# Kernel tuning notes

Hardware: AMD Instinct MI355X
Metric: run time of the kernel (lower is better)

Reference implementation:

```python
import jax, jax.numpy as jnp
import numpy as np

B = 64
N_CTRL_PLANES = 512
CPD = 64          # control_plane_dim
NF = 256          # n_frames
WS = 512          # window_size (SSM per-frame output size)
SD = 128          # state_dim
NS = NF * WS // 2 # 65536 output samples (overlap-add hop = WS//2)
TOP_K = 8


def setup_inputs() -> dict:
    key = jax.random.key(0)
    ks = jax.random.split(key, 8)
    return {
        "control_plane_choice": jax.random.normal(ks[0], (B, N_CTRL_PLANES), dtype=jnp.float32),
        "times": jax.random.normal(ks[1], (B, 1, NF), dtype=jnp.float32),
        # Lookup.items, initialized uniform(-1, 1)
        "lookup_items": jax.random.uniform(ks[2], (N_CTRL_PLANES, CPD * NF), dtype=jnp.float32, minval=-1.0, maxval=1.0),
        # SSM parameters, initialized uniform(-0.01, 0.01)
        "proj": jax.random.uniform(ks[3], (CPD, WS), dtype=jnp.float32, minval=-0.01, maxval=0.01),
        "state_matrix": jax.random.uniform(ks[4], (SD, SD), dtype=jnp.float32, minval=-0.01, maxval=0.01),
        "input_matrix": jax.random.uniform(ks[5], (WS, SD), dtype=jnp.float32, minval=-0.01, maxval=0.01),
        "output_matrix": jax.random.uniform(ks[6], (SD, WS), dtype=jnp.float32, minval=-0.01, maxval=0.01),
        "direct_matrix": jax.random.uniform(ks[7], (WS, WS), dtype=jnp.float32, minval=-0.01, maxval=0.01),
    }


def _sparse_softmax_onehot(x, axis=-1):
    # softmax then hard one-hot at the argmax with value 1 (normalize=True variant)
    sm = jax.nn.softmax(x, axis=axis)
    return (sm == jnp.max(sm, axis=axis, keepdims=True)).astype(x.dtype)


def _fft_convolve(a, b):
    # linear convolution via zero-padding to 2N, truncated back to N
    n = a.shape[-1]
    fa = jnp.fft.rfft(jnp.pad(a, ((0, 0), (0, 0), (0, n))), axis=-1)
    fb = jnp.fft.rfft(jnp.pad(b, ((0, 0), (0, 0), (0, n))), axis=-1)
    return jnp.fft.irfft(fa * fb, axis=-1)[..., :n]


def reference(control_plane_choice, times, lookup_items, proj, state_matrix, input_matrix, output_matrix, direct_matrix):
    batch = control_plane_choice.shape[0]
    cpd, ws = proj.shape
    nf = lookup_items.shape[1] // cpd
    sd = state_matrix.shape[0]
    hop = ws // 2
    ns = nf * hop

    # --- Lookup with sparse_softmax selection (hard one-hot @ items) ---
    sel = _sparse_softmax_onehot(control_plane_choice, axis=-1)   # (B, n_items)
    cp = sel @ lookup_items                                       # (B, cpd*nf)

    # --- softmax over flattened control plane, then top-8 sparsify ---
    cp = jax.nn.softmax(cp, axis=-1)                              # (B, cpd*nf)
    vals, idx = jax.lax.top_k(cp, TOP_K)                          # (B, 8)
    cp = jnp.zeros_like(cp).at[jnp.arange(batch)[:, None], idx].set(vals)
    cp = cp.reshape(batch, cpd, nf)

    # --- windowed SSM: linear state-space recurrence over frames ---
    inp = jnp.einsum('bcf,cw->fbw', cp, proj)                     # (nf, B, ws)

    def step(state, x):  # state: (B, sd), x: (B, ws)
        state = state @ state_matrix + x @ input_matrix
        out = state @ output_matrix + x @ direct_matrix
        return state, out

    state0 = jnp.zeros((batch, sd), dtype=cp.dtype)
    _, outs = jax.lax.scan(step, state0, inp)                     # (nf, B, ws)
    frames = jnp.transpose(outs, (1, 0, 2))                       # (B, nf, ws)

    # --- overlap-add with Hann window, hop = ws//2 ---
    n_ = jnp.arange(ws, dtype=cp.dtype)
    window = 0.5 * (1.0 - jnp.cos(2.0 * jnp.pi * n_ / ws))        # periodic Hann
    win_frames = frames * window
    oa_idx = jnp.arange(nf)[:, None] * hop + jnp.arange(ws)[None, :]
    sig = jnp.zeros((batch, nf * hop + ws), dtype=cp.dtype).at[:, oa_idx].add(win_frames)
    samples = sig[:, :ns][:, None, :]                             # (B, 1, ns)

    # --- Dirac scheduler: one-hot times -> upsample with holes -> fft convolve ---
    t_oh = _sparse_softmax_onehot(times, axis=-1)                 # (B, 1, nf)
    factor = ns // nf
    impulses = jnp.zeros((batch, 1, ns), dtype=cp.dtype).at[:, :, ::factor].set(t_oh)
    return _fft_convolve(samples, impulses)                       # (B, 1, ns)
```

## Files before the change

### kernel.cpp

```cpp
#include <hip/hip_runtime.h>
#include <math.h>

#define NBATCH 64
#define NCP    512
#define CPD    64
#define NF     256
#define WSZ    512
#define SD     128
#define NSAMP  65536
#define TPROP  8
#define NSLICE 8
#define SLICE_ELEMS 2048

__device__ __forceinline__ bool better(float v1, int i1, float v2, int i2) {
  return (v1 > v2) || (v1 == v2 && i1 < i2);
}

__device__ __forceinline__ void cswap(float& v1, int& i1, float& v2, int& i2) {
  if (better(v2, i2, v1, i1)) {
    float tv = v1; v1 = v2; v2 = tv;
    int   ti = i1; i1 = i2; i2 = ti;
  }
}

__device__ __forceinline__ void wave_argmax(float& v, int& i) {
#pragma unroll
  for (int off = 32; off > 0; off >>= 1) {
    float ov = __shfl_down(v, off);
    int   oi = __shfl_down(i, off);
    if (better(ov, oi, v, i)) { v = ov; i = oi; }
  }
}

__device__ __forceinline__ void xor_merge8(float* m, int* mi, int off) {
  float lb[8]; int ib8[8];
#pragma unroll
  for (int k = 0; k < 8; k++) { lb[k] = __shfl_xor(m[k], off); ib8[k] = __shfl_xor(mi[k], off); }
  float x[8]; int xi[8];
#pragma unroll
  for (int k = 0; k < 8; k++) {
    const bool ta = better(m[k], mi[k], lb[7 - k], ib8[7 - k]);
    x[k]  = ta ? m[k]  : lb[7 - k];
    xi[k] = ta ? mi[k] : ib8[7 - k];
  }
  cswap(x[0], xi[0], x[4], xi[4]); cswap(x[1], xi[1], x[5], xi[5]);
  cswap(x[2], xi[2], x[6], xi[6]); cswap(x[3], xi[3], x[7], xi[7]);
  cswap(x[0], xi[0], x[2], xi[2]); cswap(x[1], xi[1], x[3], xi[3]);
  cswap(x[4], xi[4], x[6], xi[6]); cswap(x[5], xi[5], x[7], xi[7]);
  cswap(x[0], xi[0], x[1], xi[1]); cswap(x[2], xi[2], x[3], xi[3]);
  cswap(x[4], xi[4], x[5], xi[5]); cswap(x[6], xi[6], x[7], xi[7]);
#pragma unroll
  for (int k = 0; k < 8; k++) { m[k] = x[k]; mi[k] = xi[k]; }
}

__global__ __launch_bounds__(256) void k_scan(
    const float* __restrict__ cpc, const float* __restrict__ times,
    const float* __restrict__ lookup,
    const float* __restrict__ proj, const float* __restrict__ Amat,
    const float* __restrict__ Bmat,
    float* __restrict__ S,
    float* __restrict__ pmax, float* __restrict__ psum,
    float* __restrict__ pcv, int* __restrict__ pci,
    int* __restrict__ pshift) {
  const int t = threadIdx.x;
  const int bid = blockIdx.x;

  __shared__ __align__(16) float Alds[SD * SD];
  __shared__ float sb[2][SD];
  __shared__ float sred[256];
  __shared__ float wred[4];
  __shared__ int   wredi[4];
  __shared__ int   sRow;
  __shared__ float wlv[32];
  __shared__ int   wli[32];
  __shared__ float sSmax;

  if (bid < CPD) {
    const int c = bid;
    for (int i = t; i < SD * SD / 4; i += 256)
      ((float4*)Alds)[i] = ((const float4*)Amat)[i];

    const int d = t & 127, h = t >> 7;
    {
      const float* Bp = Bmat + (size_t)(h * 256) * SD + d;
      const float* pv = proj + (size_t)c * WSZ + h * 256;
      float acc[16];
#pragma unroll
      for (int k = 0; k < 16; k++) acc[k] = 0.f;
#pragma unroll 2
      for (int kb = 0; kb < 256; kb += 16) {
#pragma unroll
        for (int u = 0; u < 16; u++)
          acc[u] = fmaf(pv[kb + u], Bp[(size_t)(kb + u) * SD], acc[u]);
      }
      float s8 = 0.f;
#pragma unroll
      for (int k = 0; k < 16; k++) s8 += acc[k];
      sred[t] = s8;
    }
    __syncthreads();
    if (t < SD) sb[0][t] = sred[t] + sred[t + 128];
    __syncthreads();

    int cur = 0;
    for (int j = 0; j < TPROP; j++) {
      if (t < SD) S[((size_t)j * CPD + c) * SD + t] = sb[cur][t];
      float a0 = 0.f, a1 = 0.f, a2 = 0.f, a3 = 0.f;
      const float* Ah = Alds + (size_t)(h * 64) * SD + d;
      const float* sh = sb[cur] + h * 64;
#pragma unroll
      for (int i = 0; i < 64; i += 4) {
        const float4 sv = *(const float4*)(sh + i);
        a0 = fmaf(sv.x, Ah[(size_t)(i + 0) * SD], a0);
        a1 = fmaf(sv.y, Ah[(size_t)(i + 1) * SD], a1);
        a2 = fmaf(sv.z, Ah[(size_t)(i + 2) * SD], a2);
        a3 = fmaf(sv.w, Ah[(size_t)(i + 3) * SD], a3);
      }
      sred[t] = (a0 + a1) + (a2 + a3);
      __syncthreads();
      if (t < SD) sb[cur ^ 1][t] = sred[t] + sred[t + 128];
      __syncthreads();
      cur ^= 1;
    }
    return;
  }

  const int sbid = bid - CPD;
  const int b = sbid >> 3, s = sbid & 7;
  const int lane = t & 63, wv = t >> 6;

  {
    float v0 = cpc[b * NCP + t];
    float v1 = cpc[b * NCP + t + 256];
    float bv = v0; int bi = t;
    if (better(v1, t + 256, bv, bi)) { bv = v1; bi = t + 256; }
    wave_argmax(bv, bi);
    if (lane == 0) { wred[wv] = bv; wredi[wv] = bi; }
    __syncthreads();
    if (t == 0) {
      float fv = wred[0]; int fi = wredi[0];
#pragma unroll
      for (int q = 1; q < 4; q++)
        if (better(wred[q], wredi[q], fv, fi)) { fv = wred[q]; fi = wredi[q]; }
      sRow = fi;
    }
    __syncthreads();
  }
  const float* row = lookup + (size_t)sRow * (CPD * NF);
  const float4* row4 = (const float4*)(row + s * SLICE_ELEMS);

  const float4 va = row4[t];
  const float4 vb = row4[t + 256];
  const int gbase = s * SLICE_ELEMS;
  float ev[8] = {va.x, va.y, va.z, va.w, vb.x, vb.y, vb.z, vb.w};
  int   ei[8] = {gbase + t * 4,        gbase + t * 4 + 1,
                 gbase + t * 4 + 2,    gbase + t * 4 + 3,
                 gbase + 1024 + t * 4, gbase + 1024 + t * 4 + 1,
                 gbase + 1024 + t * 4 + 2, gbase + 1024 + t * 4 + 3};

  float m[8]; int mi[8];
#pragma unroll
  for (int k = 0; k < 8; k++) { m[k] = ev[k]; mi[k] = ei[k]; }
#pragma unroll
  for (int i = 0; i < 7; i++)
#pragma unroll
    for (int j = 0; j < 7 - i; j++) cswap(m[j], mi[j], m[j + 1], mi[j + 1]);

  xor_merge8(m, mi, 1);  xor_merge8(m, mi, 2);  xor_merge8(m, mi, 4);
  xor_merge8(m, mi, 8);  xor_merge8(m, mi, 16); xor_merge8(m, mi, 32);

  if (lane < 8) { wlv[wv * 8 + lane] = m[lane]; wli[wv * 8 + lane] = mi[lane]; }
  __syncthreads();

  if (wv == 0) {
    float v = (lane < 32) ? wlv[lane] : -3.4e38f;
    int   i = (lane < 32) ? wli[lane] : 0x7fffffff;
#pragma unroll
    for (int k = 2; k <= 32; k <<= 1) {
#pragma unroll
      for (int j = k >> 1; j > 0; j >>= 1) {
        const float pv = __shfl_xor(v, j);
        const int   pi = __shfl_xor(i, j);
        const bool keepBetter = (((lane & k) == 0) == ((lane & j) == 0));
        if (keepBetter == better(pv, pi, v, i)) { v = pv; i = pi; }
      }
    }
    if (lane == 0) sSmax = v;
    if (lane < 8) { pcv[b * 64 + s * 8 + lane] = v; pci[b * 64 + s * 8 + lane] = i; }
  }
  __syncthreads();
  const float smax = sSmax;

  float se = 0.f;
#pragma unroll
  for (int k = 0; k < 8; k++) se += __expf(ev[k] - smax);
#pragma unroll
  for (int off = 32; off > 0; off >>= 1) se += __shfl_down(se, off);
  if (lane == 0) wred[wv] = se;
  __syncthreads();
  if (t == 0) {
    pmax[b * 8 + s] = smax;
    psum[b * 8 + s] = (wred[0] + wred[1]) + (wred[2] + wred[3]);
  }

  if (s == 0) {
    float tv = times[b * NF + t]; int ti = t;
    wave_argmax(tv, ti);
    if (lane == 0) { wred[wv] = tv; wredi[wv] = ti; }
    __syncthreads();
    if (t == 0) {
      float fv = wred[0]; int fi = wredi[0];
#pragma unroll
      for (int q = 1; q < 4; q++)
        if (better(wred[q], wredi[q], fv, fi)) { fv = wred[q]; fi = wredi[q]; }
      pshift[b] = fi * (NSAMP / NF);
    }
  }
}

__global__ __launch_bounds__(256) void k_expand(
    const float* __restrict__ proj, const float* __restrict__ Cmat,
    const float* __restrict__ Dmat, const float* __restrict__ S,
    const float* __restrict__ pmax, const float* __restrict__ psum,
    const float* __restrict__ pcv, const int* __restrict__ pci,
    float* __restrict__ P2, float* __restrict__ R,
    float* __restrict__ vals, int* __restrict__ cidx, int* __restrict__ fidx) {
  const int t = threadIdx.x;
  const int bid = blockIdx.x;
  __shared__ __align__(16) float xsh[4 * WSZ];

  if (bid < CPD / 4 * 2) {
    const int g = bid >> 1;
    const int wbase = (bid & 1) * 256;
    for (int i = t; i < 4 * WSZ; i += 256) xsh[i] = proj[(size_t)(4 * g) * WSZ + i];
    __syncthreads();
    float a0 = 0.f, a1 = 0.f, a2 = 0.f, a3 = 0.f;
    const float* Dp = Dmat + wbase + t;
#pragma unroll 8
    for (int u = 0; u < WSZ; u++) {
      const float dv = Dp[(size_t)u * WSZ];
      a0 = fmaf(xsh[u], dv, a0);
      a1 = fmaf(xsh[WSZ + u], dv, a1);
      a2 = fmaf(xsh[2 * WSZ + u], dv, a2);
      a3 = fmaf(xsh[3 * WSZ + u], dv, a3);
    }
    P2[(size_t)(4 * g + 0) * WSZ + wbase + t] = a0;
    P2[(size_t)(4 * g + 1) * WSZ + wbase + t] = a1;
    P2[(size_t)(4 * g + 2) * WSZ + wbase + t] = a2;
    P2[(size_t)(4 * g + 3) * WSZ + wbase + t] = a3;
  } else if (bid < 32 + TPROP * CPD / 4 * 2) {
    const int rb = bid - 32;
    const int g = rb >> 1;
    const int wbase = (rb & 1) * 256;
    for (int i = t; i < 4 * SD; i += 256) xsh[i] = S[(size_t)(4 * g) * SD + i];
    __syncthreads();
    float a0 = 0.f, a1 = 0.f, a2 = 0.f, a3 = 0.f;
    const float* Cp = Cmat + wbase + t;
#pragma unroll 8
    for (int i = 0; i < SD; i++) {
      const float cv = Cp[(size_t)i * WSZ];
      a0 = fmaf(xsh[i], cv, a0);
      a1 = fmaf(xsh[SD + i], cv, a1);
      a2 = fmaf(xsh[2 * SD + i], cv, a2);
      a3 = fmaf(xsh[3 * SD + i], cv, a3);
    }
    R[(size_t)(4 * g + 0) * WSZ + wbase + t] = a0;
    R[(size_t)(4 * g + 1) * WSZ + wbase + t] = a1;
    R[(size_t)(4 * g + 2) * WSZ + wbase + t] = a2;
    R[(size_t)(4 * g + 3) * WSZ + wbase + t] = a3;
  } else {
    const int b = bid - (32 + TPROP * CPD / 4 * 2);
    if (t < 64) {
      const int sl = t >> 3;
      float M = pmax[b * 8 + sl];
#pragma unroll
      for (int off = 1; off < 64; off <<= 1) M = fmaxf(M, __shfl_xor(M, off));
      float ps = ((t & 7) == 0) ? psum[b * 8 + sl] * __expf(pmax[b * 8 + sl] - M) : 0.f;
#pragma unroll
      for (int off = 1; off < 64; off <<= 1) ps += __shfl_xor(ps, off);
      float cvv = pcv[b * 64 + t]; int cii = pci[b * 64 + t];
      for (int p = 0; p < 8; p++) {
        float v = cvv; int i = cii;
#pragma unroll
        for (int off = 1; off < 64; off <<= 1) {
          float ov = __shfl_xor(v, off); int oi = __shfl_xor(i, off);
          if (better(ov, oi, v, i)) { v = ov; i = oi; }
        }
        if (t == 0) {
          vals[b * 8 + p] = __expf(v - M) / ps;
          cidx[b * 8 + p] = i / NF;
          fidx[b * 8 + p] = i % NF;
        }
        if (cii == i) cvv = -3.4e38f;
      }
    }
  }
}

__global__ __launch_bounds__(256) void k_out(
    const float* __restrict__ vals, const int* __restrict__ cidx,
    const int* __restrict__ fidx, const int* __restrict__ pshift,
    const float* __restrict__ P2, const float* __restrict__ R,
    float* __restrict__ out) {
  const int b = blockIdx.x >> 6;
  const int chunk = blockIdx.x & 63;
  const int t = threadIdx.x;
  const int n = chunk * 1024 + t * 4;
  const int m = n - pshift[b];
  float o[4] = {0.f, 0.f, 0.f, 0.f};
  if (m >= 0) {
    const int f1 = m >> 8;
    const int w1 = m & 255;
    float a[4] = {0.f, 0.f, 0.f, 0.f};
    float g[4] = {0.f, 0.f, 0.f, 0.f};
    const bool hasf2 = (f1 > 0);
#pragma unroll
    for (int k = 0; k < 8; k++) {
      const float v = vals[b * 8 + k];
      const int c = cidx[b * 8 + k];
      const int d1 = f1 - fidx[b * 8 + k];
      if (d1 >= 0 && d1 < TPROP) {
        const float4 q = *(const float4*)(R + ((size_t)(d1 * CPD + c)) * WSZ + w1);
        a[0] += v * q.x; a[1] += v * q.y; a[2] += v * q.z; a[3] += v * q.w;
      }
      if (d1 == 0) {
        const float4 q = *(const float4*)(P2 + (size_t)c * WSZ + w1);
        a[0] += v * q.x; a[1] += v * q.y; a[2] += v * q.z; a[3] += v * q.w;
      }
      if (hasf2) {
        const int d2 = d1 - 1;
        if (d2 >= 0 && d2 < TPROP) {
          const float4 q = *(const float4*)(R + ((size_t)(d2 * CPD + c)) * WSZ + w1 + 256);
          g[0] += v * q.x; g[1] += v * q.y; g[2] += v * q.z; g[3] += v * q.w;
        }
        if (d2 == 0) {
          const float4 q = *(const float4*)(P2 + (size_t)c * WSZ + w1 + 256);
          g[0] += v * q.x; g[1] += v * q.y; g[2] += v * q.z; g[3] += v * q.w;
        }
      }
    }
    const float k2pi = 6.283185307179586f / (float)WSZ;
#pragma unroll
    for (int i = 0; i < 4; i++) {
      const float cs = __cosf(k2pi * (float)(w1 + i));
      const float wa = 0.5f * (1.f - cs);
      const float wb = 0.5f * (1.f + cs);
      o[i] = wa * a[i] + wb * g[i];
    }
  }
  float4 ov = make_float4(o[0], o[1], o[2], o[3]);
  *(float4*)(out + (size_t)b * NSAMP + n) = ov;
}

extern "C" void kernel_launch(void* const* d_in, const int* in_sizes, int n_in,
                              void* d_out, int out_size, void* d_ws, size_t ws_size,
                              hipStream_t stream) {
  const float* cpc    = (const float*)d_in[0];
  const float* times  = (const float*)d_in[1];
  const float* lookup = (const float*)d_in[2];
  const float* proj   = (const float*)d_in[3];
  const float* Amat   = (const float*)d_in[4];
  const float* Bmat   = (const float*)d_in[5];
  const float* Cmat   = (const float*)d_in[6];
  const float* Dmat   = (const float*)d_in[7];
  float* out = (float*)d_out;

  float* w      = (float*)d_ws;
  float* vals   = w;
  int*   cidx   = (int*)(w + 512);
  int*   fidx   = (int*)(w + 1024);
  int*   pshift = (int*)(w + 1536);
  float* P2     = w + 1600;
  float* R      = P2 + CPD * WSZ;
  float* S      = R + (size_t)TPROP * CPD * WSZ;
  float* pmax   = S + (size_t)TPROP * CPD * SD;
  float* psum   = pmax + NBATCH * NSLICE;
  float* pcv    = psum + NBATCH * NSLICE;
  int*   pci    = (int*)(pcv + NBATCH * NSLICE * 8);

  hipLaunchKernelGGL(k_scan, dim3(CPD + NBATCH * NSLICE), dim3(256), 0, stream,
                     cpc, times, lookup, proj, Amat, Bmat,
                     S, pmax, psum, pcv, pci, pshift);
  hipLaunchKernelGGL(k_expand, dim3(32 + TPROP * CPD / 4 * 2 + NBATCH), dim3(256), 0, stream,
                     proj, Cmat, Dmat, S, pmax, psum, pcv, pci,
                     P2, R, vals, cidx, fidx);
  hipLaunchKernelGGL(k_out, dim3(NBATCH * 64), dim3(256), 0, stream,
                     vals, cidx, fidx, pshift, P2, R, out);
}
```

Before: 140.6 us.

## Fuse expand stage into scan and output kernels, dropping a launch

Removes the middle k_expand kernel. The state-to-output projection R is now computed inside the scan blocks from states kept in shared memory, and the direct projection P2 is computed by the otherwise-idle selection blocks. The final top-k merge moves into the start of every k_out block. This saves one launch and the global round trip for S, and the A matrix is now read from global memory instead of being staged in LDS. In exchange, each of the 4096 output blocks repeats the top-k merge, and the 64 scan blocks take on serial R work.

```diff
diff --git a/kernel.cpp b/kernel.cpp
--- a/kernel.cpp
+++ b/kernel.cpp
@@ -57,15 +57,16 @@
     const float* __restrict__ cpc, const float* __restrict__ times,
     const float* __restrict__ lookup,
     const float* __restrict__ proj, const float* __restrict__ Amat,
-    const float* __restrict__ Bmat,
-    float* __restrict__ S,
+    const float* __restrict__ Bmat, const float* __restrict__ Cmat,
+    const float* __restrict__ Dmat,
+    float* __restrict__ P2, float* __restrict__ R,
     float* __restrict__ pmax, float* __restrict__ psum,
     float* __restrict__ pcv, int* __restrict__ pci,
     int* __restrict__ pshift) {
   const int t = threadIdx.x;
   const int bid = blockIdx.x;
 
-  __shared__ __align__(16) float Alds[SD * SD];
+  __shared__ __align__(16) float sjall[SD * 8];
   __shared__ float sb[2][SD];
   __shared__ float sred[256];
   __shared__ float wred[4];
@@ -77,9 +78,6 @@
 
   if (bid < CPD) {
     const int c = bid;
-    for (int i = t; i < SD * SD / 4; i += 256)
-      ((float4*)Alds)[i] = ((const float4*)Amat)[i];
-
     const int d = t & 127, h = t >> 7;
     {
       const float* Bp = Bmat + (size_t)(h * 256) * SD + d;
@@ -104,9 +102,9 @@
 
     int cur = 0;
     for (int j = 0; j < TPROP; j++) {
-      if (t < SD) S[((size_t)j * CPD + c) * SD + t] = sb[cur][t];
+      if (t < SD) sjall[t * 8 + j] = sb[cur][t];
       float a0 = 0.f, a1 = 0.f, a2 = 0.f, a3 = 0.f;
-      const float* Ah = Alds + (size_t)(h * 64) * SD + d;
+      const float* Ah = Amat + (size_t)(h * 64) * SD + d;
       const float* sh = sb[cur] + h * 64;
 #pragma unroll
       for (int i = 0; i < 64; i += 4) {
@@ -121,6 +119,31 @@
       if (t < SD) sb[cur ^ 1][t] = sred[t] + sred[t + 128];
       __syncthreads();
       cur ^= 1;
+    }
+
+    float r0[8], r1[8];
+#pragma unroll
+    for (int k = 0; k < 8; k++) { r0[k] = 0.f; r1[k] = 0.f; }
+    const float* Cp = Cmat + t;
+#pragma unroll 4
+    for (int i = 0; i < SD; i++) {
+      const float4 sA = *(const float4*)(sjall + i * 8);
+      const float4 sB = *(const float4*)(sjall + i * 8 + 4);
+      const float c0 = Cp[(size_t)i * WSZ];
+      const float c1 = Cp[(size_t)i * WSZ + 256];
+      r0[0] = fmaf(sA.x, c0, r0[0]); r1[0] = fmaf(sA.x, c1, r1[0]);
+      r0[1] = fmaf(sA.y, c0, r0[1]); r1[1] = fmaf(sA.y, c1, r1[1]);
+      r0[2] = fmaf(sA.z, c0, r0[2]); r1[2] = fmaf(sA.z, c1, r1[2]);
+      r0[3] = fmaf(sA.w, c0, r0[3]); r1[3] = fmaf(sA.w, c1, r1[3]);
+      r0[4] = fmaf(sB.x, c0, r0[4]); r1[4] = fmaf(sB.x, c1, r1[4]);
+      r0[5] = fmaf(sB.y, c0, r0[5]); r1[5] = fmaf(sB.y, c1, r1[5]);
+      r0[6] = fmaf(sB.z, c0, r0[6]); r1[6] = fmaf(sB.z, c1, r1[6]);
+      r0[7] = fmaf(sB.w, c0, r0[7]); r1[7] = fmaf(sB.w, c1, r1[7]);
+    }
+#pragma unroll
+    for (int j = 0; j < 8; j++) {
+      R[((size_t)j * CPD + c) * WSZ + t]       = r0[j];
+      R[((size_t)j * CPD + c) * WSZ + t + 256] = r1[j];
     }
     return;
   }
@@ -202,6 +225,7 @@
     pmax[b * 8 + s] = smax;
     psum[b * 8 + s] = (wred[0] + wred[1]) + (wred[2] + wred[3]);
   }
+  __syncthreads();
 
   if (s == 0) {
     float tv = times[b * NF + t]; int ti = t;
@@ -216,95 +240,70 @@
       pshift[b] = fi * (NSAMP / NF);
     }
   }
-}
-
-__global__ __launch_bounds__(256) void k_expand(
-    const float* __restrict__ proj, const float* __restrict__ Cmat,
-    const float* __restrict__ Dmat, const float* __restrict__ S,
+
+  if (sbid < 256) {
+    const int c2 = sbid >> 2, q = sbid & 3;
+    const int col = q * 128 + (t & 127);
+    const int uh = t >> 7;
+    const float* pr = proj + (size_t)c2 * WSZ + uh * 256;
+    const float* Dp = Dmat + (size_t)(uh * 256) * WSZ + col;
+    float a[8];
+#pragma unroll
+    for (int k = 0; k < 8; k++) a[k] = 0.f;
+#pragma unroll 2
+    for (int u = 0; u < 256; u += 8) {
+#pragma unroll
+      for (int v = 0; v < 8; v++)
+        a[v] = fmaf(pr[u + v], Dp[(size_t)(u + v) * WSZ], a[v]);
+    }
+    float acc = 0.f;
+#pragma unroll
+    for (int k = 0; k < 8; k++) acc += a[k];
+    sred[t] = acc;
+    __syncthreads();
+    if (t < 128) P2[(size_t)c2 * WSZ + q * 128 + t] = sred[t] + sred[t + 128];
+  }
+}
+
+__global__ __launch_bounds__(256) void k_out(
     const float* __restrict__ pmax, const float* __restrict__ psum,
     const float* __restrict__ pcv, const int* __restrict__ pci,
-    float* __restrict__ P2, float* __restrict__ R,
-    float* __restrict__ vals, int* __restrict__ cidx, int* __restrict__ fidx) {
-  const int t = threadIdx.x;
-  const int bid = blockIdx.x;
-  __shared__ __align__(16) float xsh[4 * WSZ];
-
-  if (bid < CPD / 4 * 2) {
-    const int g = bid >> 1;
-    const int wbase = (bid & 1) * 256;
-    for (int i = t; i < 4 * WSZ; i += 256) xsh[i] = proj[(size_t)(4 * g) * WSZ + i];
-    __syncthreads();
-    float a0 = 0.f, a1 = 0.f, a2 = 0.f, a3 = 0.f;
-    const float* Dp = Dmat + wbase + t;
-#pragma unroll 8
-    for (int u = 0; u < WSZ; u++) {
-      const float dv = Dp[(size_t)u * WSZ];
-      a0 = fmaf(xsh[u], dv, a0);
-      a1 = fmaf(xsh[WSZ + u], dv, a1);
-      a2 = fmaf(xsh[2 * WSZ + u], dv, a2);
-      a3 = fmaf(xsh[3 * WSZ + u], dv, a3);
-    }
-    P2[(size_t)(4 * g + 0) * WSZ + wbase + t] = a0;
-    P2[(size_t)(4 * g + 1) * WSZ + wbase + t] = a1;
-    P2[(size_t)(4 * g + 2) * WSZ + wbase + t] = a2;
-    P2[(size_t)(4 * g + 3) * WSZ + wbase + t] = a3;
-  } else if (bid < 32 + TPROP * CPD / 4 * 2) {
-    const int rb = bid - 32;
-    const int g = rb >> 1;
-    const int wbase = (rb & 1) * 256;
-    for (int i = t; i < 4 * SD; i += 256) xsh[i] = S[(size_t)(4 * g) * SD + i];
-    __syncthreads();
-    float a0 = 0.f, a1 = 0.f, a2 = 0.f, a3 = 0.f;
-    const float* Cp = Cmat + wbase + t;
-#pragma unroll 8
-    for (int i = 0; i < SD; i++) {
-      const float cv = Cp[(size_t)i * WSZ];
-      a0 = fmaf(xsh[i], cv, a0);
-      a1 = fmaf(xsh[SD + i], cv, a1);
-      a2 = fmaf(xsh[2 * SD + i], cv, a2);
-      a3 = fmaf(xsh[3 * SD + i], cv, a3);
-    }
-    R[(size_t)(4 * g + 0) * WSZ + wbase + t] = a0;
-    R[(size_t)(4 * g + 1) * WSZ + wbase + t] = a1;
-    R[(size_t)(4 * g + 2) * WSZ + wbase + t] = a2;
-    R[(size_t)(4 * g + 3) * WSZ + wbase + t] = a3;
-  } else {
-    const int b = bid - (32 + TPROP * CPD / 4 * 2);
-    if (t < 64) {
-      const int sl = t >> 3;
-      float M = pmax[b * 8 + sl];
-#pragma unroll
-      for (int off = 1; off < 64; off <<= 1) M = fmaxf(M, __shfl_xor(M, off));
-      float ps = ((t & 7) == 0) ? psum[b * 8 + sl] * __expf(pmax[b * 8 + sl] - M) : 0.f;
-#pragma unroll
-      for (int off = 1; off < 64; off <<= 1) ps += __shfl_xor(ps, off);
-      float cvv = pcv[b * 64 + t]; int cii = pci[b * 64 + t];
-      for (int p = 0; p < 8; p++) {
-        float v = cvv; int i = cii;
-#pragma unroll
-        for (int off = 1; off < 64; off <<= 1) {
-          float ov = __shfl_xor(v, off); int oi = __shfl_xor(i, off);
-          if (better(ov, oi, v, i)) { v = ov; i = oi; }
-        }
-        if (t == 0) {
-          vals[b * 8 + p] = __expf(v - M) / ps;
-          cidx[b * 8 + p] = i / NF;
-          fidx[b * 8 + p] = i % NF;
-        }
-        if (cii == i) cvv = -3.4e38f;
-      }
-    }
-  }
-}
-
-__global__ __launch_bounds__(256) void k_out(
-    const float* __restrict__ vals, const int* __restrict__ cidx,
-    const int* __restrict__ fidx, const int* __restrict__ pshift,
+    const int* __restrict__ pshift,
     const float* __restrict__ P2, const float* __restrict__ R,
     float* __restrict__ out) {
   const int b = blockIdx.x >> 6;
   const int chunk = blockIdx.x & 63;
   const int t = threadIdx.x;
+  __shared__ float lv[8];
+  __shared__ int   lc[8];
+  __shared__ int   lf[8];
+
+  if (t < 64) {
+    const int sl = t >> 3;
+    float M = pmax[b * 8 + sl];
+#pragma unroll
+    for (int off = 1; off < 64; off <<= 1) M = fmaxf(M, __shfl_xor(M, off));
+    float ps = ((t & 7) == 0) ? psum[b * 8 + sl] * __expf(pmax[b * 8 + sl] - M) : 0.f;
+#pragma unroll
+    for (int off = 1; off < 64; off <<= 1) ps += __shfl_xor(ps, off);
+    float cvv = pcv[b * 64 + t]; int cii = pci[b * 64 + t];
+    for (int p = 0; p < 8; p++) {
+      float v = cvv; int i = cii;
+#pragma unroll
+      for (int off = 1; off < 64; off <<= 1) {
+        float ov = __shfl_xor(v, off); int oi = __shfl_xor(i, off);
+        if (better(ov, oi, v, i)) { v = ov; i = oi; }
+      }
+      if (t == 0) {
+        lv[p] = __expf(v - M) / ps;
+        lc[p] = i / NF;
+        lf[p] = i % NF;
+      }
+      if (cii == i) cvv = -3.4e38f;
+    }
+  }
+  __syncthreads();
+
   const int n = chunk * 1024 + t * 4;
   const int m = n - pshift[b];
   float o[4] = {0.f, 0.f, 0.f, 0.f};
@@ -316,9 +315,9 @@
     const bool hasf2 = (f1 > 0);
 #pragma unroll
     for (int k = 0; k < 8; k++) {
-      const float v = vals[b * 8 + k];
-      const int c = cidx[b * 8 + k];
-      const int d1 = f1 - fidx[b * 8 + k];
+      const float v = lv[k];
+      const int c = lc[k];
+      const int d1 = f1 - lf[k];
       if (d1 >= 0 && d1 < TPROP) {
         const float4 q = *(const float4*)(R + ((size_t)(d1 * CPD + c)) * WSZ + w1);
         a[0] += v * q.x; a[1] += v * q.y; a[2] += v * q.z; a[3] += v * q.w;
@@ -366,24 +365,18 @@
   float* out = (float*)d_out;
 
   float* w      = (float*)d_ws;
-  float* vals   = w;
-  int*   cidx   = (int*)(w + 512);
-  int*   fidx   = (int*)(w + 1024);
   int*   pshift = (int*)(w + 1536);
   float* P2     = w + 1600;
   float* R      = P2 + CPD * WSZ;
-  float* S      = R + (size_t)TPROP * CPD * WSZ;
-  float* pmax   = S + (size_t)TPROP * CPD * SD;
+  float* S_unused = R + (size_t)TPROP * CPD * WSZ;
+  float* pmax   = S_unused + (size_t)TPROP * CPD * SD;
   float* psum   = pmax + NBATCH * NSLICE;
   float* pcv    = psum + NBATCH * NSLICE;
   int*   pci    = (int*)(pcv + NBATCH * NSLICE * 8);
 
   hipLaunchKernelGGL(k_scan, dim3(CPD + NBATCH * NSLICE), dim3(256), 0, stream,
-                     cpc, times, lookup, proj, Amat, Bmat,
-                     S, pmax, psum, pcv, pci, pshift);
-  hipLaunchKernelGGL(k_expand, dim3(32 + TPROP * CPD / 4 * 2 + NBATCH), dim3(256), 0, stream,
-                     proj, Cmat, Dmat, S, pmax, psum, pcv, pci,
-                     P2, R, vals, cidx, fidx);
+                     cpc, times, lookup, proj, Amat, Bmat, Cmat, Dmat,
+                     P2, R, pmax, psum, pcv, pci, pshift);
   hipLaunchKernelGGL(k_out, dim3(NBATCH * 64), dim3(256), 0, stream,
-                     vals, cidx, fidx, pshift, P2, R, out);
-}
+                     pmax, psum, pcv, pci, pshift, P2, R, out);
+}
```

After: 129.2 us. -8.1%, faster.
